# Performance work log

Hardware: AMD Instinct MI355X
Metric: run time of the kernel (lower is better)

## Reference

```python
import jax, jax.numpy as jnp
import numpy as np

B, S, D, K = 8, 4096, 256, 8192
BETA = 0.25


def setup_inputs() -> dict:
    key = jax.random.key(0)
    k1, k2 = jax.random.split(key)
    return {
        "z": jax.random.normal(k1, (B, S, D), dtype=jnp.float32),
        "embed": jax.random.normal(k2, (K, D), dtype=jnp.float32),
    }


def reference(z, embed):
    # Inference-path VQ-EMA forward (EMA buffer updates are a no-grad side
    # effect only active in training mode; excluded from the pure reference).
    num_codes, dim = embed.shape
    z_flat = z.reshape(-1, dim)                      # [N, D]
    # squared-euclidean distances: ||z||^2 - 2 z.e^T + ||e||^2  -> [N, K]
    dist = ((z_flat * z_flat).sum(1, keepdims=True)
            - 2.0 * (z_flat @ embed.T)
            + (embed * embed).sum(1)[None, :])
    idx = jnp.argmin(dist, axis=1)                   # [N]
    z_q = embed[idx].reshape(z.shape)                # gather instead of onehot @ embed
    # commitment loss: beta * mse(stop_grad(z_q), z)
    loss = BETA * jnp.mean(jnp.square(jax.lax.stop_gradient(z_q) - z))
    # straight-through estimator
    z_q_st = z + jax.lax.stop_gradient(z_q - z)
    # perplexity from code usage histogram (scatter-add instead of onehot.mean)
    counts = jnp.zeros((num_codes,), dtype=z.dtype).at[idx].add(1.0)
    avg_probs = counts / idx.shape[0]
    perplexity = jnp.exp(-jnp.sum(avg_probs * jnp.log(avg_probs + 1e-12)))
    return z_q_st, loss, perplexity, idx.reshape(z.shape[:-1])
```

## Files before the change

### kernel.cpp

```cpp
#include <hip/hip_runtime.h>
#include <stdint.h>
#include <math.h>

#define NROWS 32768
#define DIM   256
#define KCODES 8192
#define BETA  0.25f
#define RSPLIT 16
#define NELEM 8388608
#define TAU 0.09375f

typedef float f32x4 __attribute__((ext_vector_type(4)));
typedef _Float16 v8h __attribute__((ext_vector_type(8)));
typedef unsigned short us4 __attribute__((ext_vector_type(4)));

__device__ inline unsigned int split1(float x) {
    _Float16 hf = (_Float16)x;
    _Float16 lf = (_Float16)(x - (float)hf);
    unsigned int h = __builtin_bit_cast(unsigned short, hf);
    unsigned int l = __builtin_bit_cast(unsigned short, lf);
    return h | (l << 16);
}

__device__ inline void gload_lds16(const void* g, void* l) {
    __builtin_amdgcn_global_load_lds(
        (const __attribute__((address_space(1))) void*)g,
        (__attribute__((address_space(3))) void*)l,
        16, 0, 0);
}

__device__ inline unsigned int fkey(float f) {
    unsigned int b = __float_as_uint(f);
    return (b & 0x80000000u) ? ~b : (b | 0x80000000u);
}

__global__ void prep_all(const float* __restrict__ z,
                         const float* __restrict__ e,
                         unsigned short* __restrict__ zhi,
                         unsigned short* __restrict__ zlo,
                         unsigned short* __restrict__ ehi,
                         unsigned short* __restrict__ elo,
                         float* __restrict__ enrm,
                         float* __restrict__ counts,
                         float* __restrict__ lossAcc,
                         int* __restrict__ flagcnt) {
    if (blockIdx.x < 8192) {
        int t = blockIdx.x * 256 + threadIdx.x;
        float4 v = reinterpret_cast<const float4*>(z)[t];
        unsigned int p0 = split1(v.x);
        unsigned int p1 = split1(v.y);
        unsigned int p2 = split1(v.z);
        unsigned int p3 = split1(v.w);
        us4 h, l;
        h[0] = (unsigned short)p0; l[0] = (unsigned short)(p0 >> 16);
        h[1] = (unsigned short)p1; l[1] = (unsigned short)(p1 >> 16);
        h[2] = (unsigned short)p2; l[2] = (unsigned short)(p2 >> 16);
        h[3] = (unsigned short)p3; l[3] = (unsigned short)(p3 >> 16);
        reinterpret_cast<us4*>(zhi)[t] = h;
        reinterpret_cast<us4*>(zlo)[t] = l;
    } else {
        int row = blockIdx.x - 8192;
        int d = threadIdx.x;
        float x = e[(size_t)row * DIM + d];
        unsigned int p = split1(x);
        ehi[(size_t)row * DIM + d] = (unsigned short)p;
        elo[(size_t)row * DIM + d] = (unsigned short)(p >> 16);
        float sq = x * x;
        #pragma unroll
        for (int off = 32; off; off >>= 1) sq += __shfl_down(sq, off);
        __shared__ float ps[4];
        if ((threadIdx.x & 63) == 0) ps[threadIdx.x >> 6] = sq;
        __syncthreads();
        if (threadIdx.x == 0) {
            enrm[row] = 0.5f * (ps[0] + ps[1] + ps[2] + ps[3]);
            counts[row] = 0.f;
            if (row == 0) { *lossAcc = 0.f; *flagcnt = 0; }
        }
    }
}

__launch_bounds__(512, 2)
__global__ void gemm_hi_fused(const unsigned short* __restrict__ zhi,
                              const unsigned short* __restrict__ ehi,
                              const float* __restrict__ enrm,
                              int* __restrict__ colidx,
                              float* __restrict__ out_idx,
                              int* __restrict__ flagcnt,
                              int* __restrict__ flaglist,
                              unsigned long long* __restrict__ rkey) {
    __shared__ __align__(16) unsigned short Bs[4][128 * 64];
    __shared__ float esL[KCODES];
    __shared__ float rvv[4][128];
    __shared__ float rv2s[4][128];
    __shared__ int   rcc[4][128];

    const int tid = threadIdx.x;
    const int w = tid >> 6, l = tid & 63;
    const int lx = l & 15, quad = l >> 4;
    const int wm = w >> 2, wn = w & 3;
    const int arow_base = blockIdx.x * 128;
    const int st_g = ((l & 7) ^ (l >> 3)) * 8;
    const int fr_lx7 = lx & 7;

    v8h af[4][8];
    #pragma unroll
    for (int mi = 0; mi < 4; ++mi) {
        const unsigned short* ap =
            zhi + (size_t)(arow_base + wm * 64 + mi * 16 + lx) * DIM + quad * 8;
        #pragma unroll
        for (int ks = 0; ks < 8; ++ks)
            af[mi][ks] = *(const v8h*)(ap + ks * 32);
    }

    #pragma unroll
    for (int j = 0; j < 4; ++j)
        gload_lds16(enrm + (j * 8 + w) * 256 + l * 4, &esL[(j * 8 + w) * 256]);

#define STAGE(BUF, SN, AO) do {                                               \
        const unsigned short* _s0 =                                           \
            ehi + (size_t)((SN) * 128 + (tid >> 3)) * DIM + (AO) + st_g;      \
        gload_lds16(_s0, &Bs[BUF][(w * 8) * 64]);                             \
        gload_lds16(_s0 + (size_t)64 * DIM, &Bs[BUF][(64 + w * 8) * 64]);     \
    } while (0)

    STAGE(0, 0, 0); STAGE(1, 0, 64); STAGE(2, 0, 128);

    float runv[16], runv2[16];
    int runc[16];
    #pragma unroll
    for (int s = 0; s < 16; ++s) {
        runv[s] = 3.0e38f; runv2[s] = 3.0e38f; runc[s] = 0x7fffffff;
    }

    for (int nt = 0; nt < 64; ++nt) {
        f32x4 acc[4][2];
        #pragma unroll
        for (int mi = 0; mi < 4; ++mi)
            #pragma unroll
            for (int ni = 0; ni < 2; ++ni) {
                f32x4 zz = {0.f, 0.f, 0.f, 0.f};
                acc[mi][ni] = zz;
            }

        #pragma unroll
        for (int bk = 0; bk < 4; ++bk) {
            const int sn = (bk == 0) ? nt : ((nt + 1) & 63);
            STAGE((bk + 3) & 3, sn, ((bk + 3) & 3) * 64);
            asm volatile("s_waitcnt vmcnt(6)" ::: "memory");
            __builtin_amdgcn_s_barrier();
            asm volatile("" ::: "memory");

            __builtin_amdgcn_s_setprio(1);
            #pragma unroll
            for (int kc = 0; kc < 2; ++kc) {
                const int gsw = ((kc * 4 + quad) ^ fr_lx7) * 8;
                v8h b0 = *(const v8h*)&Bs[bk][(wn * 32 + lx) * 64 + gsw];
                v8h b1 = *(const v8h*)&Bs[bk][(wn * 32 + 16 + lx) * 64 + gsw];
                #pragma unroll
                for (int mi = 0; mi < 4; ++mi) {
                    acc[mi][0] = __builtin_amdgcn_mfma_f32_16x16x32_f16(
                        af[mi][bk * 2 + kc], b0, acc[mi][0], 0, 0, 0);
                    acc[mi][1] = __builtin_amdgcn_mfma_f32_16x16x32_f16(
                        af[mi][bk * 2 + kc], b1, acc[mi][1], 0, 0, 0);
                }
            }
            __builtin_amdgcn_s_setprio(0);

            asm volatile("" ::: "memory");
            __builtin_amdgcn_s_barrier();
        }

        const int cb = nt * 128 + wn * 32 + lx;
        #pragma unroll
        for (int ni = 0; ni < 2; ++ni) {
            const int col = cb + ni * 16;
            const float es = esL[col];
            #pragma unroll
            for (int mi = 0; mi < 4; ++mi)
                #pragma unroll
                for (int r = 0; r < 4; ++r) {
                    const int s = mi * 4 + r;
                    const float sv = es - acc[mi][ni][r];
                    const bool lt = sv < runv[s];
                    runv2[s] = __builtin_amdgcn_fmed3f(sv, runv[s], runv2[s]);
                    runc[s] = lt ? col : runc[s];
                    runv[s] = fminf(runv[s], sv);
                }
        }
    }
#undef STAGE

    #pragma unroll
    for (int s = 0; s < 16; ++s) {
        float v1 = runv[s], v2 = runv2[s];
        int c1 = runc[s];
        #pragma unroll
        for (int m = 1; m < 16; m <<= 1) {
            float ov1 = __shfl_xor(v1, m);
            int oc1 = __shfl_xor(c1, m);
            float ov2 = __shfl_xor(v2, m);
            float mx = fmaxf(v1, ov1);
            v2 = fminf(fminf(v2, ov2), mx);
            bool take = (ov1 < v1) || (ov1 == v1 && oc1 < c1);
            v1 = take ? ov1 : v1;
            c1 = take ? oc1 : c1;
        }
        if (lx == 0) {
            const int rl = wm * 64 + (s >> 2) * 16 + quad * 4 + (s & 3);
            rvv[wn][rl] = v1; rcc[wn][rl] = c1; rv2s[wn][rl] = v2;
        }
    }
    __syncthreads();
    if (tid < 128) {
        float v1 = rvv[0][tid], v2 = rv2s[0][tid];
        int c1 = rcc[0][tid];
        #pragma unroll
        for (int q = 1; q < 4; ++q) {
            float ov1 = rvv[q][tid], ov2 = rv2s[q][tid];
            int oc1 = rcc[q][tid];
            float mx = fmaxf(v1, ov1);
            v2 = fminf(fminf(v2, ov2), mx);
            bool take = (ov1 < v1) || (ov1 == v1 && oc1 < c1);
            v1 = take ? ov1 : v1;
            c1 = take ? oc1 : c1;
        }
        const int row = arow_base + tid;
        out_idx[row] = (float)c1;
        if (v2 - v1 < TAU) {
            int slot = atomicAdd(flagcnt, 1);
            flaglist[slot] = row;
            rkey[slot] = ~0ull;
            colidx[row] = -(slot + 1);
        } else {
            colidx[row] = c1;
        }
    }
}

__launch_bounds__(256, 2)
__global__ void rescue_gemm(const unsigned short* __restrict__ zhi,
                            const unsigned short* __restrict__ zlo,
                            const unsigned short* __restrict__ ehi,
                            const unsigned short* __restrict__ elo,
                            const float* __restrict__ enrm,
                            const int* __restrict__ flagcnt,
                            const int* __restrict__ flaglist,
                            unsigned long long* __restrict__ rkey) {
    __shared__ __align__(16) unsigned short As[128 * 64];
    __shared__ __align__(16) unsigned short Bs[128 * 64];
    __shared__ float rv[2][128];
    __shared__ int   rc[2][128];

    const int count = *flagcnt;
    const int tid = threadIdx.x;
    const int w = tid >> 6, l = tid & 63;
    const int lx = l & 15, quad = l >> 4;
    const int wm = w >> 1, wn = w & 1;
    const int cs = blockIdx.y;
    const int cbase_cs = cs * (KCODES / RSPLIT);

    const int st_row8 = l >> 3;
    const int st_g = (((l & 7) ^ (l >> 3)) * 8);
    const int fr_lx7 = lx & 7;

    for (int tb = blockIdx.x * 128; tb < count; tb += 32 * 128) {
        int arowj[4];
        #pragma unroll
        for (int j = 0; j < 4; ++j) {
            int li = tb + w * 32 + j * 8 + st_row8;
            arowj[j] = (li < count) ? flaglist[li] : 0;
        }

        float runv[16];
        int runc[16];
        #pragma unroll
        for (int s = 0; s < 16; ++s) { runv[s] = 3.0e38f; runc[s] = 0x7fffffff; }

        for (int nt = 0; nt < (KCODES / RSPLIT) / 128; ++nt) {
            const int colbase = cbase_cs + nt * 128;
            f32x4 acc[4][4];
            #pragma unroll
            for (int mi = 0; mi < 4; ++mi)
                #pragma unroll
                for (int ni = 0; ni < 4; ++ni) {
                    f32x4 zz = {0.f, 0.f, 0.f, 0.f};
                    acc[mi][ni] = zz;
                }

            #pragma unroll
            for (int seg = 0; seg < 3; ++seg) {
                const unsigned short* za = (seg == 2) ? zlo : zhi;
                const unsigned short* eb = (seg == 1) ? elo : ehi;
                for (int bk = 0; bk < 4; ++bk) {
                    const int ao = bk * 64;
                    __syncthreads();
                    #pragma unroll
                    for (int j = 0; j < 4; ++j) {
                        const int r = w * 32 + j * 8 + st_row8;
                        gload_lds16(za + (size_t)arowj[j] * DIM + ao + st_g,
                                    &As[(w * 32 + j * 8) * 64]);
                        gload_lds16(eb + (size_t)(colbase + r) * DIM + ao + st_g,
                                    &Bs[(w * 32 + j * 8) * 64]);
                    }
                    __syncthreads();
                    #pragma unroll
                    for (int kc = 0; kc < 2; ++kc) {
                        const int gsw = ((kc * 4 + quad) ^ fr_lx7) * 8;
                        v8h af[4], bfr[4];
                        #pragma unroll
                        for (int mi = 0; mi < 4; ++mi)
                            af[mi] = *(const v8h*)&As[(wm * 64 + mi * 16 + lx) * 64 + gsw];
                        #pragma unroll
                        for (int ni = 0; ni < 4; ++ni)
                            bfr[ni] = *(const v8h*)&Bs[(wn * 64 + ni * 16 + lx) * 64 + gsw];
                        #pragma unroll
                        for (int mi = 0; mi < 4; ++mi)
                            #pragma unroll
                            for (int ni = 0; ni < 4; ++ni)
                                acc[mi][ni] = __builtin_amdgcn_mfma_f32_16x16x32_f16(
                                    af[mi], bfr[ni], acc[mi][ni], 0, 0, 0);
                    }
                }
            }

            #pragma unroll
            for (int ni = 0; ni < 4; ++ni) {
                const int col = colbase + wn * 64 + ni * 16 + lx;
                const float es = enrm[col];
                #pragma unroll
                for (int mi = 0; mi < 4; ++mi)
                    #pragma unroll
                    for (int r = 0; r < 4; ++r) {
                        float sv = es - acc[mi][ni][r];
                        const int s = mi * 4 + r;
                        if (sv < runv[s]) { runv[s] = sv; runc[s] = col; }
                    }
            }
        }

        #pragma unroll
        for (int s = 0; s < 16; ++s) {
            float v = runv[s]; int c = runc[s];
            #pragma unroll
            for (int m = 1; m < 16; m <<= 1) {
                float ov = __shfl_xor(v, m);
                int oc = __shfl_xor(c, m);
                if (ov < v || (ov == v && oc < c)) { v = ov; c = oc; }
            }
            if (lx == 0) {
                const int mi = s >> 2, r = s & 3;
                const int rl = wm * 64 + mi * 16 + quad * 4 + r;
                rv[wn][rl] = v; rc[wn][rl] = c;
            }
        }
        __syncthreads();
        if (tid < 128) {
            float v0 = rv[0][tid]; int c0 = rc[0][tid];
            float v1 = rv[1][tid]; int c1 = rc[1][tid];
            if (v1 < v0 || (v1 == v0 && c1 < c0)) { v0 = v1; c0 = c1; }
            const int li = tb + tid;
            if (li < count) {
                unsigned long long key =
                    ((unsigned long long)fkey(v0) << 32) | (unsigned int)c0;
                atomicMin(&rkey[li], key);
            }
        }
        __syncthreads();
    }
}

__global__ void fused_out(const int* __restrict__ colidx,
                          const unsigned long long* __restrict__ rkey,
                          const float* __restrict__ z,
                          const float* __restrict__ embed,
                          float* __restrict__ out_zq,
                          float* __restrict__ out_idx,
                          float* __restrict__ counts,
                          float* __restrict__ lossAcc) {
    __shared__ int cidx[16];
    const int tid = threadIdx.x;
    if (tid < 16) {
        const int row = blockIdx.x * 16 + tid;
        int c = colidx[row];
        if (c < 0) {
            c = (int)(unsigned int)(rkey[-c - 1] & 0x1FFFull);
            out_idx[row] = (float)c;
        }
        cidx[tid] = c;
        atomicAdd(&counts[c], 1.0f);
    }
    __syncthreads();
    const int d = tid;
    float ls = 0.f;
    #pragma unroll 4
    for (int i = 0; i < 16; ++i) {
        const int row = blockIdx.x * 16 + i;
        const int c = cidx[i];
        const float zv = z[(size_t)row * DIM + d];
        const float ev = embed[(size_t)c * DIM + d];
        const float diff = ev - zv;
        out_zq[(size_t)row * DIM + d] = zv + diff;
        ls += diff * diff;
    }
    #pragma unroll
    for (int off = 32; off; off >>= 1) ls += __shfl_down(ls, off);
    __shared__ float ps[4];
    if ((tid & 63) == 0) ps[tid >> 6] = ls;
    __syncthreads();
    if (tid == 0) atomicAdd(lossAcc, ps[0] + ps[1] + ps[2] + ps[3]);
}

__global__ void finalize(const float* __restrict__ counts,
                         const float* __restrict__ lossAcc,
                         float* __restrict__ out_loss,
                         float* __restrict__ out_perp) {
    float h = 0.f;
    for (int k = threadIdx.x; k < KCODES; k += 256) {
        float p = counts[k] * (1.0f / (float)NROWS);
        h += p * logf(p + 1e-12f);
    }
    #pragma unroll
    for (int off = 32; off; off >>= 1) h += __shfl_down(h, off);
    __shared__ float ps[4];
    if ((threadIdx.x & 63) == 0) ps[threadIdx.x >> 6] = h;
    __syncthreads();
    if (threadIdx.x == 0) {
        *out_perp = expf(-(ps[0] + ps[1] + ps[2] + ps[3]));
        *out_loss = BETA * lossAcc[0] / (float)NELEM;
    }
}

extern "C" void kernel_launch(void* const* d_in, const int* in_sizes, int n_in,
                              void* d_out, int out_size, void* d_ws, size_t ws_size,
                              hipStream_t stream) {
    const float* z = (const float*)d_in[0];
    const float* embed = (const float*)d_in[1];
    char* ws = (char*)d_ws;

    unsigned short* zhi = (unsigned short*)(ws + 0);
    unsigned short* zlo = (unsigned short*)(ws + 16777216);
    unsigned short* ehi = (unsigned short*)(ws + 33554432);
    unsigned short* elo = (unsigned short*)(ws + 37748736);
    float* enrm    = (float*)(ws + 41943040);
    int*   colidx  = (int*)  (ws + 43548672);
    float* counts  = (float*)(ws + 43679744);
    float* lossAcc = (float*)(ws + 43712512);
    int*   flagcnt = (int*)  (ws + 43712516);
    int*   flaglist = (int*) (ws + 43712520);
    unsigned long long* rkey = (unsigned long long*)(ws + 43843592);

    float* out = (float*)d_out;
    float* out_zq   = out;
    float* out_loss = out + 8388608;
    float* out_perp = out + 8388609;
    float* out_idx  = out + 8388610;

    prep_all<<<16384, 256, 0, stream>>>(z, embed, zhi, zlo, ehi, elo, enrm,
                                        counts, lossAcc, flagcnt);
    gemm_hi_fused<<<NROWS / 128, 512, 0, stream>>>(
        zhi, ehi, enrm, colidx, out_idx, flagcnt, flaglist, rkey);
    rescue_gemm<<<dim3(32, RSPLIT), 256, 0, stream>>>(
        zhi, zlo, ehi, elo, enrm, flagcnt, flaglist, rkey);
    fused_out<<<NROWS / 16, 256, 0, stream>>>(colidx, rkey, z, embed,
                                              out_zq, out_idx, counts, lossAcc);
    finalize<<<1, 256, 0, stream>>>(counts, lossAcc, out_loss, out_perp);
}
```

Baseline: 344.8 us.

## Widen GEMM K-stages to 128, seed accumulators with code norms

Restructures the main distance GEMM so each LDS stage covers 128 K-elements instead of 64, giving two barrier-fenced MFMA phases per N-tile instead of four. The accumulator is now initialised with the negated half code norm loaded directly from global memory, so the epilogue tracks a running max and no longer subtracts per element or needs an LDS copy of all norms. The aim is fewer barriers and waitcnts per tile and less epilogue ALU work, at the cost of a larger LDS footprint (128 KB of B buffers), which may reduce occupancy below the declared two blocks per CU.

Result: slower. 352.4 us (+2.2%).

```diff
diff --git a/kernel.cpp b/kernel.cpp
--- a/kernel.cpp
+++ b/kernel.cpp
@@ -88,8 +88,7 @@
                               int* __restrict__ flagcnt,
                               int* __restrict__ flaglist,
                               unsigned long long* __restrict__ rkey) {
-    __shared__ __align__(16) unsigned short Bs[4][128 * 64];
-    __shared__ float esL[KCODES];
+    __shared__ __align__(16) unsigned short Bs[4][128 * 128];
     __shared__ float rvv[4][128];
     __shared__ float rv2s[4][128];
     __shared__ int   rcc[4][128];
@@ -99,8 +98,11 @@
     const int lx = l & 15, quad = l >> 4;
     const int wm = w >> 2, wn = w & 3;
     const int arow_base = blockIdx.x * 128;
-    const int st_g = ((l & 7) ^ (l >> 3)) * 8;
     const int fr_lx7 = lx & 7;
+    const int ecol = wn * 32 + lx;
+
+    const int st_row = w * 4 + (l >> 4);
+    const int st_sw = ((l & 15) ^ (st_row & 7)) * 8;
 
     v8h af[4][8];
     #pragma unroll
@@ -112,118 +114,131 @@
             af[mi][ks] = *(const v8h*)(ap + ks * 32);
     }
 
-    #pragma unroll
-    for (int j = 0; j < 4; ++j)
-        gload_lds16(enrm + (j * 8 + w) * 256 + l * 4, &esL[(j * 8 + w) * 256]);
-
-#define STAGE(BUF, SN, AO) do {                                               \
-        const unsigned short* _s0 =                                           \
-            ehi + (size_t)((SN) * 128 + (tid >> 3)) * DIM + (AO) + st_g;      \
-        gload_lds16(_s0, &Bs[BUF][(w * 8) * 64]);                             \
-        gload_lds16(_s0 + (size_t)64 * DIM, &Bs[BUF][(64 + w * 8) * 64]);     \
-    } while (0)
-
-    STAGE(0, 0, 0); STAGE(1, 0, 64); STAGE(2, 0, 128);
-
-    float runv[16], runv2[16];
+#define STAGE(BUF, CNT, KB) do {                                              \
+        const unsigned short* _s = ehi                                        \
+            + (((size_t)(CNT) * 128 + st_row) << 8) + (KB) * 128 + st_sw;     \
+        unsigned short* _d = &Bs[BUF][(w * 4) * 128];                         \
+        gload_lds16(_s,             _d);                                      \
+        gload_lds16(_s + (32 << 8), _d + 32 * 128);                           \
+        gload_lds16(_s + (64 << 8), _d + 64 * 128);                           \
+        gload_lds16(_s + (96 << 8), _d + 96 * 128);                           \
+} while (0)
+
+#define FENCE_MFMA(BUF, BK) do {                                              \
+        asm volatile("s_waitcnt vmcnt(14)" ::: "memory");                     \
+        __builtin_amdgcn_s_barrier();                                         \
+        asm volatile("" ::: "memory");                                        \
+        __builtin_amdgcn_s_setprio(1);                                        \
+        _Pragma("unroll") for (int kc = 0; kc < 4; ++kc) {                    \
+            const int gsw = ((kc * 4 + quad) ^ fr_lx7) * 8;                   \
+            v8h b0 = *(const v8h*)&Bs[BUF][(wn * 32 + lx) * 128 + gsw];       \
+            v8h b1 = *(const v8h*)&Bs[BUF][(wn * 32 + 16 + lx) * 128 + gsw];  \
+            _Pragma("unroll") for (int mi = 0; mi < 4; ++mi) {                \
+                acc[mi][0] = __builtin_amdgcn_mfma_f32_16x16x32_f16(          \
+                    af[mi][(BK) * 4 + kc], b0, acc[mi][0], 0, 0, 0);          \
+                acc[mi][1] = __builtin_amdgcn_mfma_f32_16x16x32_f16(          \
+                    af[mi][(BK) * 4 + kc], b1, acc[mi][1], 0, 0, 0);          \
+            }                                                                 \
+        }                                                                     \
+        __builtin_amdgcn_s_setprio(0);                                        \
+        asm volatile("" ::: "memory");                                        \
+        __builtin_amdgcn_s_barrier();                                         \
+} while (0)
+
+#define EPILOGUE(NT) do {                                                     \
+        _Pragma("unroll") for (int ni = 0; ni < 2; ++ni) {                    \
+            const int col = (NT) * 128 + ecol + ni * 16;                      \
+            _Pragma("unroll") for (int mi = 0; mi < 4; ++mi)                  \
+                _Pragma("unroll") for (int r = 0; r < 4; ++r) {               \
+                    const int s = mi * 4 + r;                                 \
+                    const float a = acc[mi][ni][r];                           \
+                    const bool gt = a > runm[s];                              \
+                    runm2[s] = __builtin_amdgcn_fmed3f(a, runm[s], runm2[s]); \
+                    runc[s] = gt ? col : runc[s];                             \
+                    runm[s] = fmaxf(runm[s], a);                              \
+                }                                                             \
+        }                                                                     \
+} while (0)
+
+#define STEP_BK0(BUF, NT) do {                                                \
+        const float a0 = -esn0, a1 = -esn1;                                   \
+        _Pragma("unroll") for (int mi = 0; mi < 4; ++mi) {                    \
+            acc[mi][0] = (f32x4){a0, a0, a0, a0};                             \
+            acc[mi][1] = (f32x4){a1, a1, a1, a1};                             \
+        }                                                                     \
+        { const int nn = ((NT) + 1) & 63;                                     \
+          esn0 = enrm[nn * 128 + ecol];                                       \
+          esn1 = enrm[nn * 128 + ecol + 16]; }                                \
+        STAGE((BUF + 3) & 3, ((NT) + 1) & 63, 1);                             \
+        FENCE_MFMA(BUF, 0);                                                   \
+} while (0)
+
+#define STEP_BK1(BUF, NT) do {                                                \
+        STAGE((BUF + 3) & 3, ((NT) + 2) & 63, 0);                             \
+        FENCE_MFMA(BUF, 1);                                                   \
+        EPILOGUE(NT);                                                         \
+} while (0)
+
+    float esn0 = enrm[ecol];
+    float esn1 = enrm[ecol + 16];
+    STAGE(0, 0, 0); STAGE(1, 0, 1); STAGE(2, 1, 0);
+
+    float runm[16], runm2[16];
     int runc[16];
     #pragma unroll
     for (int s = 0; s < 16; ++s) {
-        runv[s] = 3.0e38f; runv2[s] = 3.0e38f; runc[s] = 0x7fffffff;
-    }
-
-    for (int nt = 0; nt < 64; ++nt) {
-        f32x4 acc[4][2];
-        #pragma unroll
-        for (int mi = 0; mi < 4; ++mi)
-            #pragma unroll
-            for (int ni = 0; ni < 2; ++ni) {
-                f32x4 zz = {0.f, 0.f, 0.f, 0.f};
-                acc[mi][ni] = zz;
-            }
-
-        #pragma unroll
-        for (int bk = 0; bk < 4; ++bk) {
-            const int sn = (bk == 0) ? nt : ((nt + 1) & 63);
-            STAGE((bk + 3) & 3, sn, ((bk + 3) & 3) * 64);
-            asm volatile("s_waitcnt vmcnt(6)" ::: "memory");
-            __builtin_amdgcn_s_barrier();
-            asm volatile("" ::: "memory");
-
-            __builtin_amdgcn_s_setprio(1);
-            #pragma unroll
-            for (int kc = 0; kc < 2; ++kc) {
-                const int gsw = ((kc * 4 + quad) ^ fr_lx7) * 8;
-                v8h b0 = *(const v8h*)&Bs[bk][(wn * 32 + lx) * 64 + gsw];
-                v8h b1 = *(const v8h*)&Bs[bk][(wn * 32 + 16 + lx) * 64 + gsw];
-                #pragma unroll
-                for (int mi = 0; mi < 4; ++mi) {
-                    acc[mi][0] = __builtin_amdgcn_mfma_f32_16x16x32_f16(
-                        af[mi][bk * 2 + kc], b0, acc[mi][0], 0, 0, 0);
-                    acc[mi][1] = __builtin_amdgcn_mfma_f32_16x16x32_f16(
-                        af[mi][bk * 2 + kc], b1, acc[mi][1], 0, 0, 0);
-                }
-            }
-            __builtin_amdgcn_s_setprio(0);
-
-            asm volatile("" ::: "memory");
-            __builtin_amdgcn_s_barrier();
-        }
-
-        const int cb = nt * 128 + wn * 32 + lx;
-        #pragma unroll
-        for (int ni = 0; ni < 2; ++ni) {
-            const int col = cb + ni * 16;
-            const float es = esL[col];
-            #pragma unroll
-            for (int mi = 0; mi < 4; ++mi)
-                #pragma unroll
-                for (int r = 0; r < 4; ++r) {
-                    const int s = mi * 4 + r;
-                    const float sv = es - acc[mi][ni][r];
-                    const bool lt = sv < runv[s];
-                    runv2[s] = __builtin_amdgcn_fmed3f(sv, runv[s], runv2[s]);
-                    runc[s] = lt ? col : runc[s];
-                    runv[s] = fminf(runv[s], sv);
-                }
-        }
+        runm[s] = -3.0e38f; runm2[s] = -3.0e38f; runc[s] = 0x7fffffff;
+    }
+
+    f32x4 acc[4][2];
+    for (int nt2 = 0; nt2 < 32; ++nt2) {
+        const int nt0 = nt2 * 2;
+        STEP_BK0(0, nt0);
+        STEP_BK1(1, nt0);
+        STEP_BK0(2, nt0 + 1);
+        STEP_BK1(3, nt0 + 1);
     }
 #undef STAGE
+#undef FENCE_MFMA
+#undef EPILOGUE
+#undef STEP_BK0
+#undef STEP_BK1
 
     #pragma unroll
     for (int s = 0; s < 16; ++s) {
-        float v1 = runv[s], v2 = runv2[s];
+        float m1 = runm[s], m2 = runm2[s];
         int c1 = runc[s];
         #pragma unroll
         for (int m = 1; m < 16; m <<= 1) {
-            float ov1 = __shfl_xor(v1, m);
-            int oc1 = __shfl_xor(c1, m);
-            float ov2 = __shfl_xor(v2, m);
-            float mx = fmaxf(v1, ov1);
-            v2 = fminf(fminf(v2, ov2), mx);
-            bool take = (ov1 < v1) || (ov1 == v1 && oc1 < c1);
-            v1 = take ? ov1 : v1;
-            c1 = take ? oc1 : c1;
+            float o1 = __shfl_xor(m1, m);
+            int oc = __shfl_xor(c1, m);
+            float o2 = __shfl_xor(m2, m);
+            float mn = fminf(m1, o1);
+            m2 = fmaxf(fmaxf(m2, o2), mn);
+            bool take = (o1 > m1) || (o1 == m1 && oc < c1);
+            m1 = take ? o1 : m1;
+            c1 = take ? oc : c1;
         }
         if (lx == 0) {
             const int rl = wm * 64 + (s >> 2) * 16 + quad * 4 + (s & 3);
-            rvv[wn][rl] = v1; rcc[wn][rl] = c1; rv2s[wn][rl] = v2;
+            rvv[wn][rl] = m1; rcc[wn][rl] = c1; rv2s[wn][rl] = m2;
         }
     }
     __syncthreads();
     if (tid < 128) {
-        float v1 = rvv[0][tid], v2 = rv2s[0][tid];
+        float m1 = rvv[0][tid], m2 = rv2s[0][tid];
         int c1 = rcc[0][tid];
         #pragma unroll
         for (int q = 1; q < 4; ++q) {
-            float ov1 = rvv[q][tid], ov2 = rv2s[q][tid];
-            int oc1 = rcc[q][tid];
-            float mx = fmaxf(v1, ov1);
-            v2 = fminf(fminf(v2, ov2), mx);
-            bool take = (ov1 < v1) || (ov1 == v1 && oc1 < c1);
-            v1 = take ? ov1 : v1;
-            c1 = take ? oc1 : c1;
-        }
+            float o1 = rvv[q][tid], o2 = rv2s[q][tid];
+            int oc = rcc[q][tid];
+            float mn = fminf(m1, o1);
+            m2 = fmaxf(fmaxf(m2, o2), mn);
+            bool take = (o1 > m1) || (o1 == m1 && oc < c1);
+            m1 = take ? o1 : m1;
+            c1 = take ? oc : c1;
+        }
+        const float v1 = -m1, v2 = -m2;
         const int row = arow_base + tid;
         out_idx[row] = (float)c1;
         if (v2 - v1 < TAU) {
```
